# Kernel tuning notes

Hardware: AMD Instinct MI355X
Metric: run time of the kernel (lower is better)

The kernel has to match this reference:

```python
import jax, jax.numpy as jnp
import numpy as np

N_USER = 150_000
M_ITEM = 30_000
N_NODES = N_USER + M_ITEM
D = 64                      # embedding_dim
N_LAYERS = 3                # gcn_layer_number
E = 600_000                 # user-item interactions (symmetric nnz = 2E)
B = 1024
NUM_RATE, NUM_GENRE, NUM_DIR, NUM_ACT = 6, 25, 2186, 8030
NUM_GENDER, NUM_AGE, NUM_OCC, NUM_ZIP = 2, 7, 21, 3402
H1, H2 = 64, 64             # first/second fc hidden dims
FC1_IN = D * 10


def setup_inputs() -> dict:
    key = jax.random.key(0)
    ks = jax.random.split(key, 24)
    # aux features: 0/1 values are valid indices for every categorical field
    aux_info = jax.random.randint(ks[0], (B, 10246), 0, 2, dtype=jnp.int32)
    user_ids = jax.random.randint(ks[1], (B,), 0, N_USER, dtype=jnp.int32)
    item_ids = jax.random.randint(ks[2], (B,), 0, M_ITEM, dtype=jnp.int32)
    # bipartite graph: random interactions, symmetric normalized adjacency
    u = jax.random.randint(ks[3], (E,), 0, N_USER, dtype=jnp.int32)
    i = jax.random.randint(ks[4], (E,), 0, M_ITEM, dtype=jnp.int32) + N_USER
    graph_row = jnp.concatenate([u, i])
    graph_col = jnpph = jnp.concatenate([i, u]) if False else jnp.concatenate([i, u])
    deg = jax.ops.segment_sum(jnp.ones((2 * E,), jnp.float32), graph_row, num_segments=N_NODES)
    dinv = jnp.where(deg > 0, jax.lax.rsqrt(jnp.maximum(deg, 1.0)), 0.0)
    graph_val = dinv[graph_row] * dinv[graph_col]
    s = 0.1
    nrm = lambda k, shp: (jax.random.normal(k, shp, jnp.float32) * s)
    return {
        "aux_info": aux_info, "user_ids": user_ids, "item_ids": item_ids,
        "graph_row": graph_row, "graph_col": graph_col, "graph_val": graph_val,
        "rate_tab": nrm(ks[5], (NUM_RATE, D)),
        "genre_W": nrm(ks[6], (NUM_GENRE, D)),
        "director_W": nrm(ks[7], (NUM_DIR, D)),
        "actor_W": nrm(ks[8], (NUM_ACT, D)),
        "gender_tab": nrm(ks[9], (NUM_GENDER, D)),
        "age_tab": nrm(ks[10], (NUM_AGE, D)),
        "occ_tab": nrm(ks[11], (NUM_OCC, D)),
        "area_tab": nrm(ks[12], (NUM_ZIP, D)),
        "user_rel": nrm(ks[13], (N_USER, D)),
        "item_rel": nrm(ks[14], (M_ITEM, D)),
        "fc1_W": nrm(ks[15], (FC1_IN, H1)), "fc1_b": jnp.zeros((H1,), jnp.float32),
        "fc2_W": nrm(ks[16], (H1, H2)), "fc2_b": jnp.zeros((H2,), jnp.float32),
        "out_W": nrm(ks[17], (H2, 1)), "out_b": jnp.zeros((1,), jnp.float32),
    }


def _lightgcn(user_rel, item_rel, row, col, val):
    # LightGCN: repeated SpMM D^-1/2 A D^-1/2 @ emb, mean over layer outputs
    emb = jnp.concatenate([user_rel, item_rel], axis=0)      # [N, D]
    acc = emb
    for _ in range(N_LAYERS):
        emb = jax.ops.segment_sum(val[:, None] * emb[col], row, num_segments=N_NODES)
        acc = acc + emb
    light = acc / (N_LAYERS + 1)
    return light[:N_USER], light[N_USER:]


def _multi_hot(idx_int, W):
    x = idx_int.astype(jnp.float32)
    return (x @ W) / jnp.sum(x, axis=1, keepdims=True)


def reference(aux_info, user_ids, item_ids, graph_row, graph_col, graph_val,
              rate_tab, genre_W, director_W, actor_W,
              gender_tab, age_tab, occ_tab, area_tab,
              user_rel, item_rel,
              fc1_W, fc1_b, fc2_W, fc2_b, out_W, out_b):
    rate_idx = aux_info[:, 0]
    genre_idx = aux_info[:, 1:26]
    director_idx = aux_info[:, 26:2212]
    actor_idx = aux_info[:, 2212:10242]
    gender_idx = aux_info[:, 10242]
    age_idx = aux_info[:, 10243]
    occ_idx = aux_info[:, 10244]
    area_idx = aux_info[:, 10245]

    item_emb = jnp.concatenate([
        rate_tab[rate_idx],
        _multi_hot(genre_idx, genre_W),
        _multi_hot(director_idx, director_W),
        _multi_hot(actor_idx, actor_W),
    ], axis=1)                                               # [B, 4D]
    user_emb = jnp.concatenate([
        gender_tab[gender_idx], age_tab[age_idx],
        occ_tab[occ_idx], area_tab[area_idx],
    ], axis=1)                                               # [B, 4D]

    all_users, all_items = _lightgcn(user_rel, item_rel, graph_row, graph_col, graph_val)
    X = jnp.concatenate([item_emb, user_emb,
                         all_users[user_ids], all_items[item_ids]], axis=1)  # [B, 10D]
    X = jax.nn.relu(X @ fc1_W + fc1_b)
    X = jax.nn.relu(X @ fc2_W + fc2_b)
    return X @ out_W + out_b                                 # [B, 1]
```

## Files before the change

### kernel.cpp

```cpp
#include <hip/hip_runtime.h>
#include <hip/hip_bf16.h>
#include <hip/hip_fp16.h>

#define N_USER 150000
#define M_ITEM 30000
#define N_NODES 180000
#define E2 1200000
#define BATCH 1024
#define AUX_W 10246
#define KP_G 32
#define KP_D 2208
#define KP_A 8064
#define NBKT 265
#define WT_BLKS 2576
#define BCNT_BLKS 293

typedef __attribute__((ext_vector_type(8))) short short8;
typedef __attribute__((ext_vector_type(4))) float f32x4;

__device__ __forceinline__ int bucket_of(int r) {
    return r < N_USER ? (r >> 10) : 147 + ((r - N_USER) >> 8);
}

__device__ __forceinline__ int detect_f32(const void* probe) {
    float v = __bfloat162float(((const __hip_bfloat16*)probe)[threadIdx.x & 63]);
    unsigned long long m = __ballot(!(fabsf(v) < 1000.0f));
    return __popcll(m) > 8;
}

struct CvtSeg { const void* src; float* dst; int n; int blk0; };
struct CvtBatch { CvtSeg seg[16]; };

__global__ void __launch_bounds__(256) k_prep(CvtBatch cb, int cvtBlks,
                                              const void* Wg, const void* Wd, const void* Wa,
                                              unsigned short* WtG, unsigned short* WtD, unsigned short* WtA,
                                              const int* __restrict__ grow, int* __restrict__ bucket_tot,
                                              const void* probe) {
    int blk = blockIdx.x, tid = threadIdx.x;
    if (blk < cvtBlks) {
        int isf32 = detect_f32(probe);
        int si = 0;
        #pragma unroll
        for (int i = 0; i < 16; ++i) if (blk >= cb.seg[i].blk0) si = i;
        const CvtSeg sg = cb.seg[si];
        int i = (blk - sg.blk0) * 256 + tid;
        if (i >= sg.n) return;
        if (isf32) sg.dst[i] = ((const float*)sg.src)[i];
        else       sg.dst[i] = __bfloat162float(((const __hip_bfloat16*)sg.src)[i]);
        return;
    }
    if (blk < cvtBlks + WT_BLKS) {
        int isf32 = detect_f32(probe);
        int t = (blk - cvtBlks) * 256 + tid;
        if (t >= (KP_G + KP_D + KP_A) * 64) return;
        int kp = t >> 6, n = t & 63;
        int k, K; const void* src; unsigned short* dst;
        if (kp < KP_G)              { k = kp;               K = 25;   src = Wg; dst = WtG; }
        else if (kp < KP_G + KP_D)  { k = kp - KP_G;        K = 2186; src = Wd; dst = WtD; }
        else                        { k = kp - KP_G - KP_D; K = 8030; src = Wa; dst = WtA; }
        unsigned short v = 0;
        if (k < K) {
            if (isf32) {
                __hip_bfloat16 h = __float2bfloat16(((const float*)src)[(size_t)k * 64 + n]);
                v = *(unsigned short*)&h;
            } else {
                v = ((const unsigned short*)src)[(size_t)k * 64 + n];
            }
        }
        dst[(((size_t)(k >> 5) * 64 + n) * 4 + ((k >> 3) & 3)) * 8 + (k & 7)] = v;
        return;
    }
    __shared__ int h[NBKT];
    for (int i = tid; i < NBKT; i += 256) h[i] = 0;
    __syncthreads();
    int idx0 = (blk - cvtBlks - WT_BLKS) * 4096;
    #pragma unroll
    for (int k = 0; k < 16; ++k) {
        int i = idx0 + k * 256 + tid;
        if (i < E2) atomicAdd(&h[bucket_of(grow[i])], 1);
    }
    __syncthreads();
    for (int i = tid; i < NBKT; i += 256) if (h[i]) atomicAdd(&bucket_tot[i], h[i]);
}

__global__ void __launch_bounds__(512) k_bscan(const int* __restrict__ bucket_tot,
                                               int* __restrict__ bucket_base,
                                               int* __restrict__ bucketcur) {
    __shared__ int s[512];
    int tid = threadIdx.x;
    s[tid] = (tid < NBKT) ? bucket_tot[tid] : 0;
    __syncthreads();
    for (int off = 1; off < 512; off <<= 1) {
        int v = (tid >= off) ? s[tid - off] : 0;
        __syncthreads();
        s[tid] += v;
        __syncthreads();
    }
    int excl = tid ? s[tid - 1] : 0;
    bucket_base[tid] = excl;
    if (tid < NBKT) bucketcur[tid] = excl;
}

__global__ void __launch_bounds__(256) k_p1(const int* __restrict__ grow, const int* __restrict__ gcol,
                                            int* __restrict__ bucketcur, int2* __restrict__ binned) {
    __shared__ int h1[NBKT], base1[NBKT];
    int tid = threadIdx.x;
    for (int i = tid; i < NBKT; i += 256) h1[i] = 0;
    __syncthreads();
    int idx0 = blockIdx.x * 4096;
    int r[16], c[16];
    #pragma unroll
    for (int k = 0; k < 16; ++k) {
        int i = idx0 + k * 256 + tid;
        if (i < E2) {
            r[k] = grow[i]; c[k] = gcol[i];
            atomicAdd(&h1[bucket_of(r[k])], 1);
        } else r[k] = -1;
    }
    __syncthreads();
    for (int i = tid; i < NBKT; i += 256) {
        base1[i] = h1[i] ? atomicAdd(&bucketcur[i], h1[i]) : 0;
        h1[i] = 0;
    }
    __syncthreads();
    #pragma unroll
    for (int k = 0; k < 16; ++k) {
        if (r[k] >= 0) {
            int b = bucket_of(r[k]);
            int p = base1[b] + atomicAdd(&h1[b], 1);
            binned[p] = make_int2(r[k], c[k]);
        }
    }
}

__global__ void __launch_bounds__(256) k_p2(const int2* __restrict__ binned, const int* __restrict__ bb,
                                            int* __restrict__ cols, int2* __restrict__ moffs,
                                            float* __restrict__ dinv, float* __restrict__ dsq,
                                            float* __restrict__ gsc) {
    __shared__ int h[1024];
    __shared__ int ws2[256];
    int b = blockIdx.x, tid = threadIdx.x;
    int r0, r1;
    if (b < 147) { r0 = b << 10; r1 = min((b + 1) << 10, N_USER); }
    else         { r0 = N_USER + ((b - 147) << 8); r1 = min(N_USER + ((b - 146) << 8), N_NODES); }
    int s0 = bb[b], e0 = bb[b + 1];
    for (int i = tid; i < 1024; i += 256) h[i] = 0;
    __syncthreads();
    for (int j = s0 + tid; j < e0; j += 256) atomicAdd(&h[binned[j].x - r0], 1);
    __syncthreads();
    int t0 = tid * 4;
    int a0 = h[t0], a1 = h[t0 + 1], a2 = h[t0 + 2], a3 = h[t0 + 3];
    ws2[tid] = a0 + a1 + a2 + a3;
    __syncthreads();
    for (int off = 1; off < 256; off <<= 1) {
        int v = (tid >= off) ? ws2[tid - off] : 0;
        __syncthreads();
        ws2[tid] += v;
        __syncthreads();
    }
    int excl = tid ? ws2[tid - 1] : 0;
    int ex[4] = { excl, excl + a0, excl + a0 + a1, excl + a0 + a1 + a2 };
    int ac[4] = { a0, a1, a2, a3 };
    #pragma unroll
    for (int i = 0; i < 4; ++i) {
        int row = r0 + t0 + i;
        if (row < r1) {
            moffs[row] = make_int2(s0 + ex[i], s0 + ex[i] + ac[i]);
            float deg = (float)ac[i];
            bool nz = deg > 0.f;
            dinv[row] = nz ? rsqrtf(deg) : 0.f;
            dsq[row]  = nz ? 1.f / deg  : 0.f;
            gsc[row]  = nz ? sqrtf(deg) : 0.f;
        }
        h[t0 + i] = ex[i];
    }
    __syncthreads();
    for (int j = s0 + tid; j < e0; j += 256) {
        int2 e = binned[j];
        int p = s0 + atomicAdd(&h[e.x - r0], 1);
        cols[p] = e.y << 7;
    }
}

__device__ void mhgemm_body(int blk, const int* __restrict__ aux,
                            const unsigned short* __restrict__ WtG,
                            const unsigned short* __restrict__ WtD,
                            const unsigned short* __restrict__ WtA,
                            float* __restrict__ Xmh, float* __restrict__ cntf) {
    int seg, rb, k0, klen, Kseg, auxoff;
    const unsigned short* Wt;
    if (blk < 16)      { seg = 0; rb = blk;                      k0 = 0;              klen = 25;                  Kseg = 25;   auxoff = 1;    Wt = WtG; }
    else if (blk < 96) { int t = blk - 16; seg = 1; rb = t & 15; k0 = (t >> 4) * 512; klen = min(512, 2186 - k0); Kseg = 2186; auxoff = 26;   Wt = WtD; }
    else               { int t = blk - 96; seg = 2; rb = t & 15; k0 = (t >> 4) * 512; klen = min(512, 8030 - k0); Kseg = 8030; auxoff = 2212; Wt = WtA; }
    int lane = threadIdx.x & 63, wave = threadIdx.x >> 6;
    int m = lane & 15, quad = lane >> 4;
    int row = rb * 64 + wave * 16 + m;
    const int* arow = aux + (size_t)row * AUX_W + auxoff;

    f32x4 acc0 = {0.f,0.f,0.f,0.f}, acc1 = acc0, acc2 = acc0, acc3 = acc0;
    float asum = 0.f;
    int nchunk = (klen + 31) >> 5;
    for (int kci = 0; kci < nchunk; ++kci) {
        int kb = k0 + kci * 32 + quad * 8;
        short8 af;
        if (kb + 8 <= Kseg) {
            #pragma unroll
            for (int j = 0; j < 8; ++j) {
                int x = arow[kb + j];
                af[j] = x ? (short)0x3F80 : (short)0;
                asum += (float)x;
            }
        } else {
            #pragma unroll
            for (int j = 0; j < 8; ++j) {
                int x = (kb + j < Kseg) ? arow[kb + j] : 0;
                af[j] = x ? (short)0x3F80 : (short)0;
                asum += (float)x;
            }
        }
        size_t kcg = (size_t)(k0 >> 5) + kci;
        const unsigned short* bp = Wt + ((kcg * 64 + m) * 4 + quad) * 8;
        short8 b0 = *(const short8*)(bp);
        short8 b1 = *(const short8*)(bp + 512);
        short8 b2 = *(const short8*)(bp + 1024);
        short8 b3 = *(const short8*)(bp + 1536);
        acc0 = __builtin_amdgcn_mfma_f32_16x16x32_bf16(af, b0, acc0, 0, 0, 0);
        acc1 = __builtin_amdgcn_mfma_f32_16x16x32_bf16(af, b1, acc1, 0, 0, 0);
        acc2 = __builtin_amdgcn_mfma_f32_16x16x32_bf16(af, b2, acc2, 0, 0, 0);
        acc3 = __builtin_amdgcn_mfma_f32_16x16x32_bf16(af, b3, acc3, 0, 0, 0);
    }
    asum += __shfl_xor(asum, 16);
    asum += __shfl_xor(asum, 32);
    if (quad == 0) atomicAdd(&cntf[seg * BATCH + row], asum);
    float* xbase = Xmh + ((size_t)seg * BATCH + rb * 64 + wave * 16 + quad * 4) * 64;
    #pragma unroll
    for (int reg = 0; reg < 4; ++reg) {
        float* xr = xbase + (size_t)reg * 64;
        atomicAdd(&xr[ 0 + m], acc0[reg]);
        atomicAdd(&xr[16 + m], acc1[reg]);
        atomicAdd(&xr[32 + m], acc2[reg]);
        atomicAdd(&xr[48 + m], acc3[reg]);
    }
}

__global__ void __launch_bounds__(256) k_cvt_fused(const void* rawU, const void* rawI,
                                                   const float* __restrict__ dinv,
                                                   __half* __restrict__ emb,
                                                   float* __restrict__ tacc,
                                                   const int* __restrict__ uids,
                                                   const int* __restrict__ iids, int cvtN,
                                                   const int2* __restrict__ moffs,
                                                   const int* __restrict__ cols,
                                                   int2* __restrict__ moffs2,
                                                   const int* __restrict__ aux,
                                                   const unsigned short* __restrict__ WtG,
                                                   const unsigned short* __restrict__ WtD,
                                                   const unsigned short* __restrict__ WtA,
                                                   float* __restrict__ Xmh, float* __restrict__ cntf) {
    int blk = blockIdx.x;
    if (blk < 352) {
        mhgemm_body(blk, aux, WtG, WtD, WtA, Xmh, cntf);
        return;
    }
    if (blk < 864) {
        int lane = threadIdx.x & 63;
        int t = (blk - 352) * 4 + (threadIdx.x >> 6);
        int r = (t < BATCH) ? uids[t] : (N_USER + iids[t - BATCH]);
        int2 se = moffs[r];
        if (lane == 0) moffs2[r] = se;
        for (int j = se.x + lane; j < se.y; j += 64) {
            int c = (unsigned)cols[j] >> 7;
            moffs2[c] = moffs[c];
        }
        return;
    }
    int isf32 = detect_f32(rawU);
    if (blk < 1376) {
        int lane = threadIdx.x & 63;
        int t = (blk - 864) * 4 + (threadIdx.x >> 6);
        const void* src; size_t ri;
        if (t < BATCH) { src = rawU; ri = (size_t)uids[t]; }
        else           { src = rawI; ri = (size_t)iids[t - BATCH]; }
        float v;
        if (isf32) v = ((const float*)src)[ri * 64 + lane];
        else       v = __bfloat162float(((const __hip_bfloat16*)src)[ri * 64 + lane]);
        tacc[(size_t)t * 64 + lane] = v;
        return;
    }
    int q = (blk - 1376) * 256 + threadIdx.x;
    if (q >= N_NODES * 16) return;
    int r = q >> 4;
    const void* src; size_t qq;
    if (r < N_USER) { src = rawU; qq = (size_t)q; }
    else            { src = rawI; qq = (size_t)q - (size_t)N_USER * 16; }
    float d = dinv[r];
    float4 v;
    if (isf32) {
        v = ((const float4*)src)[qq];
    } else {
        ushort4 u = ((const ushort4*)src)[qq];
        v.x = __bfloat162float(*(__hip_bfloat16*)&u.x);
        v.y = __bfloat162float(*(__hip_bfloat16*)&u.y);
        v.z = __bfloat162float(*(__hip_bfloat16*)&u.z);
        v.w = __bfloat162float(*(__hip_bfloat16*)&u.w);
    }
    __half h0 = __float2half(v.x * d), h1 = __float2half(v.y * d);
    __half h2 = __float2half(v.z * d), h3 = __float2half(v.w * d);
    ushort4 o = { *(unsigned short*)&h0, *(unsigned short*)&h1,
                  *(unsigned short*)&h2, *(unsigned short*)&h3 };
    ((ushort4*)emb)[(size_t)q] = o;
}

__global__ void __launch_bounds__(256, 8) k_spmv(const __half* __restrict__ src, __half* __restrict__ dst,
                                                 const int2* __restrict__ moffs_in, const int* __restrict__ cols,
                                                 const float* __restrict__ dsq,
                                                 int spmvN, float* __restrict__ tacc,
                                                 const int* __restrict__ uids, const int* __restrict__ iids,
                                                 const float* __restrict__ gsc) {
    int tid = threadIdx.x, lane = tid & 63;
    int blk = blockIdx.x;
    if (blk >= spmvN) {
        int t = (blk - spmvN) * 4 + (tid >> 6);
        int r = (t < BATCH) ? uids[t] : (N_USER + iids[t - BATCH]);
        tacc[(size_t)t * 64 + lane] += __half2float(src[(size_t)r * 64 + lane]) * gsc[r];
        return;
    }
    int wid = blk * 4 + (tid >> 6);
    if (wid >= N_NODES) return;
    int2 se = moffs_in[wid];
    int s = se.x, e = se.y;
    if (e <= s) return;
    int p = lane & 31, ep = lane >> 5;
    const char* sb = (const char*)src + (p << 2);
    float ax = 0.f, ay = 0.f;
    int j0 = s;
    for (; j0 + 16 <= e; j0 += 16) {
        int c[8];
        #pragma unroll
        for (int u = 0; u < 8; ++u) c[u] = cols[j0 + 2 * u + ep];
        float2 v[8];
        #pragma unroll
        for (int u = 0; u < 8; ++u) v[u] = __half22float2(*(const __half2*)(sb + (size_t)(unsigned)c[u]));
        #pragma unroll
        for (int u = 0; u < 8; ++u) { ax += v[u].x; ay += v[u].y; }
    }
    if (j0 + 8 <= e) {
        int c[4];
        #pragma unroll
        for (int u = 0; u < 4; ++u) c[u] = cols[j0 + 2 * u + ep];
        float2 v[4];
        #pragma unroll
        for (int u = 0; u < 4; ++u) v[u] = __half22float2(*(const __half2*)(sb + (size_t)(unsigned)c[u]));
        #pragma unroll
        for (int u = 0; u < 4; ++u) { ax += v[u].x; ay += v[u].y; }
        j0 += 8;
    }
    if (j0 + 4 <= e) {
        int c0 = cols[j0 + ep], c1 = cols[j0 + 2 + ep];
        float2 v0 = __half22float2(*(const __half2*)(sb + (size_t)(unsigned)c0));
        float2 v1 = __half22float2(*(const __half2*)(sb + (size_t)(unsigned)c1));
        ax += v0.x + v1.x; ay += v0.y + v1.y;
        j0 += 4;
    }
    if (j0 < e) {
        int j1 = j0 + ep, j2 = j0 + 2 + ep;
        int c0 = cols[min(j1, e - 1)], c1 = cols[min(j2, e - 1)];
        float w0 = (j1 < e) ? 1.f : 0.f, w1 = (j2 < e) ? 1.f : 0.f;
        float2 v0 = __half22float2(*(const __half2*)(sb + (size_t)(unsigned)c0));
        float2 v1 = __half22float2(*(const __half2*)(sb + (size_t)(unsigned)c1));
        ax = fmaf(w0, v0.x, ax); ay = fmaf(w0, v0.y, ay);
        ax = fmaf(w1, v1.x, ax); ay = fmaf(w1, v1.y, ay);
    }
    ax += __shfl_xor(ax, 32);
    ay += __shfl_xor(ay, 32);
    if (ep == 0) {
        float d = dsq[wid];
        *(__half2*)((char*)dst + ((size_t)wid << 7) + (p << 2)) = __floats2half2_rn(ax * d, ay * d);
    }
}

__global__ void __launch_bounds__(256) k_spmv3(const __half* __restrict__ src, float* __restrict__ tacc,
                                               const int2* __restrict__ moffs, const int* __restrict__ cols,
                                               const float* __restrict__ dinv, const float* __restrict__ gsc,
                                               const int* __restrict__ uids, const int* __restrict__ iids) {
    int tid = threadIdx.x, lane = tid & 63;
    int t = blockIdx.x * 4 + (tid >> 6);
    if (t >= 2048) return;
    int r = (t < BATCH) ? uids[t] : (N_USER + iids[t - BATCH]);
    int2 se = moffs[r];
    int s = se.x, e = se.y;
    int p = lane & 31, ep = lane >> 5;
    const char* sb = (const char*)src + (p << 2);
    float ax = 0.f, ay = 0.f;
    int j0 = s;
    for (; j0 + 16 <= e; j0 += 16) {
        int c[8];
        #pragma unroll
        for (int u = 0; u < 8; ++u) c[u] = cols[j0 + 2 * u + ep];
        float2 v[8];
        #pragma unroll
        for (int u = 0; u < 8; ++u) v[u] = __half22float2(*(const __half2*)(sb + (size_t)(unsigned)c[u]));
        #pragma unroll
        for (int u = 0; u < 8; ++u) { ax += v[u].x; ay += v[u].y; }
    }
    if (j0 + 8 <= e) {
        int c[4];
        #pragma unroll
        for (int u = 0; u < 4; ++u) c[u] = cols[j0 + 2 * u + ep];
        float2 v[4];
        #pragma unroll
        for (int u = 0; u < 4; ++u) v[u] = __half22float2(*(const __half2*)(sb + (size_t)(unsigned)c[u]));
        #pragma unroll
        for (int u = 0; u < 4; ++u) { ax += v[u].x; ay += v[u].y; }
        j0 += 8;
    }
    if (j0 + 4 <= e) {
        int c0 = cols[j0 + ep], c1 = cols[j0 + 2 + ep];
        float2 v0 = __half22float2(*(const __half2*)(sb + (size_t)(unsigned)c0));
        float2 v1 = __half22float2(*(const __half2*)(sb + (size_t)(unsigned)c1));
        ax += v0.x + v1.x; ay += v0.y + v1.y;
        j0 += 4;
    }
    if (j0 < e) {
        int j1 = j0 + ep, j2 = j0 + 2 + ep;
        int c0 = cols[min(j1, e - 1)], c1 = cols[min(j2, e - 1)];
        float w0 = (j1 < e) ? 1.f : 0.f, w1 = (j2 < e) ? 1.f : 0.f;
        float2 v0 = __half22float2(*(const __half2*)(sb + (size_t)(unsigned)c0));
        float2 v1 = __half22float2(*(const __half2*)(sb + (size_t)(unsigned)c1));
        ax = fmaf(w0, v0.x, ax); ay = fmaf(w0, v0.y, ay);
        ax = fmaf(w1, v1.x, ax); ay = fmaf(w1, v1.y, ay);
    }
    ax += __shfl_xor(ax, 32);
    ay += __shfl_xor(ay, 32);
    if (ep == 0) {
        float2 self = __half22float2(*(const __half2*)((const char*)src + ((size_t)r << 7) + (p << 2)));
        float di = dinv[r], g = gsc[r];
        float* tp = tacc + (size_t)t * 64 + (p << 1);
        tp[0] += di * ax + g * self.x;
        tp[1] += di * ay + g * self.y;
    }
}

__global__ void __launch_bounds__(256) k_mlp(const int* __restrict__ aux,
                                             const float* __restrict__ ratef, const float* __restrict__ genderf,
                                             const float* __restrict__ agef, const float* __restrict__ occf,
                                             const float* __restrict__ areaf, const float* __restrict__ tacc,
                                             const float* __restrict__ Xmh, const float* __restrict__ cntf,
                                             const float* __restrict__ W1, const float* __restrict__ b1,
                                             const float* __restrict__ W2, const float* __restrict__ b2,
                                             const float* __restrict__ Wo, const float* __restrict__ bo,
                                             void* __restrict__ out, const void* probe) {
    __shared__ float sx[4][640];
    __shared__ float sh[4][64];
    int isf32 = detect_f32(probe);
    int lane = threadIdx.x & 63, w = threadIdx.x >> 6;
    int b = blockIdx.x * 4 + w;
    const int* arow = aux + (size_t)b * AUX_W;
    float* xr = sx[w];
    xr[0   + lane] = ratef[arow[0] * 64 + lane];
    xr[64  + lane] = Xmh[((size_t)0 * BATCH + b) * 64 + lane] / cntf[0 * BATCH + b];
    xr[128 + lane] = Xmh[((size_t)1 * BATCH + b) * 64 + lane] / cntf[1 * BATCH + b];
    xr[192 + lane] = Xmh[((size_t)2 * BATCH + b) * 64 + lane] / cntf[2 * BATCH + b];
    xr[256 + lane] = genderf[arow[10242] * 64 + lane];
    xr[320 + lane] = agef[arow[10243] * 64 + lane];
    xr[384 + lane] = occf[arow[10244] * 64 + lane];
    xr[448 + lane] = areaf[arow[10245] * 64 + lane];
    xr[512 + lane] = tacc[(size_t)b * 64 + lane] * 0.25f;
    xr[576 + lane] = tacc[(size_t)(BATCH + b) * 64 + lane] * 0.25f;
    float acc = b1[lane];
    #pragma unroll 8
    for (int k = 0; k < 640; ++k) acc += xr[k] * W1[(size_t)k * 64 + lane];
    float h1 = fmaxf(acc, 0.f);
    sh[w][lane] = h1;
    float acc2 = b2[lane];
    #pragma unroll 8
    for (int j = 0; j < 64; ++j) acc2 += sh[w][j] * W2[(size_t)j * 64 + lane];
    float h2 = fmaxf(acc2, 0.f);
    float p = h2 * Wo[lane];
    #pragma unroll
    for (int off = 32; off; off >>= 1) p += __shfl_down(p, off);
    if (lane == 0) {
        float r = p + bo[0];
        if (isf32) ((float*)out)[b] = r;
        else       ((__hip_bfloat16*)out)[b] = __float2bfloat16(r);
    }
}

extern "C" void kernel_launch(void* const* d_in, const int* in_sizes, int n_in,
                              void* d_out, int out_size, void* d_ws, size_t ws_size,
                              hipStream_t stream) {
    const int* aux  = (const int*)d_in[0];
    const int* uids = (const int*)d_in[1];
    const int* iids = (const int*)d_in[2];
    const int* grow = (const int*)d_in[3];
    const int* gcol = (const int*)d_in[4];

    char* p = (char*)d_ws;
    auto alloc = [&](size_t bytes) -> char* {
        char* r = p;
        p += (bytes + 255) / 256 * 256;
        return r;
    };
    int*   bucket_tot  = (int*)alloc(512 * 4);
    float* Xmh         = (float*)alloc((size_t)3 * BATCH * 64 * 4);
    float* cntf        = (float*)alloc((size_t)3 * BATCH * 4);
    int2*  moffs2      = (int2*)alloc((size_t)180224 * 8);
    char*  zero_end    = p;
    int*   bucket_base = (int*)alloc(512 * 4);
    int*   bucketcur   = (int*)alloc(512 * 4);
    int2*  moffs       = (int2*)alloc((size_t)180224 * 8);
    float* dinv        = (float*)alloc((size_t)180224 * 4);
    float* dsq         = (float*)alloc((size_t)180224 * 4);
    float* gsc         = (float*)alloc((size_t)180224 * 4);
    int2*  binned      = (int2*)alloc((size_t)E2 * 8);
    int*   cols        = (int*)alloc((size_t)E2 * 4);
    __half* embA       = (__half*)alloc((size_t)N_NODES * 64 * 2);
    __half* embB       = (__half*)alloc((size_t)N_NODES * 64 * 2);
    float* tacc        = (float*)alloc((size_t)2048 * 64 * 4);
    unsigned short* WtG = (unsigned short*)alloc((size_t)KP_G * 64 * 2);
    unsigned short* WtD = (unsigned short*)alloc((size_t)KP_D * 64 * 2);
    unsigned short* WtA = (unsigned short*)alloc((size_t)KP_A * 64 * 2);
    float* ratef   = (float*)alloc(384 * 4);
    float* genderf = (float*)alloc(128 * 4);
    float* agef    = (float*)alloc(448 * 4);
    float* occf    = (float*)alloc(1344 * 4);
    float* areaf   = (float*)alloc((size_t)217728 * 4);
    float* fc1W    = (float*)alloc((size_t)40960 * 4);
    float* fc1b    = (float*)alloc(64 * 4);
    float* fc2W    = (float*)alloc(4096 * 4);
    float* fc2b    = (float*)alloc(64 * 4);
    float* outW    = (float*)alloc(64 * 4);
    float* outb    = (float*)alloc(4);

    const void* probe = d_in[14];

    hipMemsetAsync(bucket_tot, 0, (size_t)(zero_end - (char*)bucket_tot), stream);

    CvtBatch cb;
    int blk = 0, si = 0;
    auto addseg = [&](const void* s, float* d, int n) {
        cb.seg[si].src = s; cb.seg[si].dst = d; cb.seg[si].n = n; cb.seg[si].blk0 = blk;
        blk += (n + 255) / 256; ++si;
    };
    addseg(d_in[6],  ratef,   384);
    addseg(d_in[10], genderf, 128);
    addseg(d_in[11], agef,    448);
    addseg(d_in[12], occf,    1344);
    addseg(d_in[13], areaf,   217728);
    addseg(d_in[16], fc1W,   40960);
    addseg(d_in[17], fc1b,   64);
    addseg(d_in[18], fc2W,   4096);
    addseg(d_in[19], fc2b,   64);
    addseg(d_in[20], outW,   64);
    addseg(d_in[21], outb,   1);
    for (int i = si; i < 16; ++i) { cb.seg[i].src = nullptr; cb.seg[i].dst = nullptr; cb.seg[i].n = 0; cb.seg[i].blk0 = 0x7fffffff; }
    const int cvtBlks = blk;
    hipLaunchKernelGGL(k_prep, dim3(cvtBlks + WT_BLKS + BCNT_BLKS), dim3(256), 0, stream,
                       cb, cvtBlks, d_in[7], d_in[8], d_in[9], WtG, WtD, WtA, grow, bucket_tot, probe);

    hipLaunchKernelGGL(k_bscan, dim3(1), dim3(512), 0, stream, bucket_tot, bucket_base, bucketcur);
    hipLaunchKernelGGL(k_p1, dim3((E2 + 4095) / 4096), dim3(256), 0, stream, grow, gcol, bucketcur, binned);
    hipLaunchKernelGGL(k_p2, dim3(NBKT), dim3(256), 0, stream, binned, bucket_base, cols, moffs, dinv, dsq, gsc);

    const int cvtN = (N_NODES * 16 + 255) / 256;
    hipLaunchKernelGGL(k_cvt_fused, dim3(1376 + cvtN), dim3(256), 0, stream,
                       d_in[14], d_in[15], dinv, embA, tacc, uids, iids, cvtN,
                       moffs, cols, moffs2, aux, WtG, WtD, WtA, Xmh, cntf);

    const int spmvN = (N_NODES + 3) / 4;
    hipLaunchKernelGGL(k_spmv, dim3(spmvN), dim3(256), 0, stream,
                       embA, embB, moffs, cols, dsq, spmvN, (float*)nullptr, uids, iids, gsc);
    hipLaunchKernelGGL(k_spmv, dim3(spmvN + 512), dim3(256), 0, stream,
                       embB, embA, moffs2, cols, dsq, spmvN, tacc, uids, iids, gsc);
    hipLaunchKernelGGL(k_spmv3, dim3(2048 / 4), dim3(256), 0, stream,
                       embA, tacc, moffs, cols, dinv, gsc, uids, iids);

    hipLaunchKernelGGL(k_mlp, dim3(BATCH / 4), dim3(256), 0, stream,
                       aux, ratef, genderf, agef, occf, areaf, tacc, Xmh, cntf,
                       fc1W, fc1b, fc2W, fc2b, outW, outb, d_out, probe);
}
```

Baseline: 335.0 us.

## Map eight rows per wavefront in SpMV with 16-byte gathers

The SpMV kernel now assigns eight graph rows to each 64-lane wavefront, with eight lanes per row each loading a 16-byte chunk (eight halves) of a neighbour embedding. This replaces the one-row-per-wave scheme that used 4-byte loads split across two half-waves plus a cross-lane shuffle. The goal is to cut wave count and use wider vector gathers, so idle lanes on short rows (average degree is about 6-7) are reduced. The tradeoff is that rows with very different degrees inside one wave can diverge, and the grid size assumes N_NODES divides evenly by 32.

```diff
diff --git a/kernel.cpp b/kernel.cpp
--- a/kernel.cpp
+++ b/kernel.cpp
@@ -325,57 +325,61 @@
         tacc[(size_t)t * 64 + lane] += __half2float(src[(size_t)r * 64 + lane]) * gsc[r];
         return;
     }
-    int wid = blk * 4 + (tid >> 6);
-    if (wid >= N_NODES) return;
-    int2 se = moffs_in[wid];
+    int wid8 = blk * 4 + (tid >> 6);
+    int g = lane >> 3, l8 = lane & 7;
+    int r = wid8 * 8 + g;
+    int2 se = moffs_in[r];
     int s = se.x, e = se.y;
-    if (e <= s) return;
-    int p = lane & 31, ep = lane >> 5;
-    const char* sb = (const char*)src + (p << 2);
-    float ax = 0.f, ay = 0.f;
+    const char* sb = (const char*)src + (l8 << 4);
+    float2 a0 = {0.f,0.f}, a1 = a0, a2 = a0, a3 = a0;
     int j0 = s;
-    for (; j0 + 16 <= e; j0 += 16) {
-        int c[8];
-        #pragma unroll
-        for (int u = 0; u < 8; ++u) c[u] = cols[j0 + 2 * u + ep];
-        float2 v[8];
-        #pragma unroll
-        for (int u = 0; u < 8; ++u) v[u] = __half22float2(*(const __half2*)(sb + (size_t)(unsigned)c[u]));
-        #pragma unroll
-        for (int u = 0; u < 8; ++u) { ax += v[u].x; ay += v[u].y; }
-    }
-    if (j0 + 8 <= e) {
+    for (; j0 + 4 <= e; j0 += 4) {
         int c[4];
         #pragma unroll
-        for (int u = 0; u < 4; ++u) c[u] = cols[j0 + 2 * u + ep];
-        float2 v[4];
-        #pragma unroll
-        for (int u = 0; u < 4; ++u) v[u] = __half22float2(*(const __half2*)(sb + (size_t)(unsigned)c[u]));
-        #pragma unroll
-        for (int u = 0; u < 4; ++u) { ax += v[u].x; ay += v[u].y; }
-        j0 += 8;
-    }
-    if (j0 + 4 <= e) {
-        int c0 = cols[j0 + ep], c1 = cols[j0 + 2 + ep];
-        float2 v0 = __half22float2(*(const __half2*)(sb + (size_t)(unsigned)c0));
-        float2 v1 = __half22float2(*(const __half2*)(sb + (size_t)(unsigned)c1));
-        ax += v0.x + v1.x; ay += v0.y + v1.y;
-        j0 += 4;
+        for (int u = 0; u < 4; ++u) c[u] = cols[j0 + u];
+        float4 rv[4];
+        #pragma unroll
+        for (int u = 0; u < 4; ++u) rv[u] = *(const float4*)(sb + (size_t)(unsigned)c[u]);
+        #pragma unroll
+        for (int u = 0; u < 4; ++u) {
+            const __half2* h = (const __half2*)&rv[u];
+            float2 f0 = __half22float2(h[0]), f1 = __half22float2(h[1]);
+            float2 f2 = __half22float2(h[2]), f3 = __half22float2(h[3]);
+            a0.x += f0.x; a0.y += f0.y; a1.x += f1.x; a1.y += f1.y;
+            a2.x += f2.x; a2.y += f2.y; a3.x += f3.x; a3.y += f3.y;
+        }
     }
     if (j0 < e) {
-        int j1 = j0 + ep, j2 = j0 + 2 + ep;
-        int c0 = cols[min(j1, e - 1)], c1 = cols[min(j2, e - 1)];
-        float w0 = (j1 < e) ? 1.f : 0.f, w1 = (j2 < e) ? 1.f : 0.f;
-        float2 v0 = __half22float2(*(const __half2*)(sb + (size_t)(unsigned)c0));
-        float2 v1 = __half22float2(*(const __half2*)(sb + (size_t)(unsigned)c1));
-        ax = fmaf(w0, v0.x, ax); ay = fmaf(w0, v0.y, ay);
-        ax = fmaf(w1, v1.x, ax); ay = fmaf(w1, v1.y, ay);
-    }
-    ax += __shfl_xor(ax, 32);
-    ay += __shfl_xor(ay, 32);
-    if (ep == 0) {
-        float d = dsq[wid];
-        *(__half2*)((char*)dst + ((size_t)wid << 7) + (p << 2)) = __floats2half2_rn(ax * d, ay * d);
+        int c[4]; float w[4];
+        #pragma unroll
+        for (int u = 0; u < 4; ++u) {
+            int j = j0 + u;
+            c[u] = cols[min(j, e - 1)];
+            w[u] = (j < e) ? 1.f : 0.f;
+        }
+        float4 rv[4];
+        #pragma unroll
+        for (int u = 0; u < 4; ++u) rv[u] = *(const float4*)(sb + (size_t)(unsigned)c[u]);
+        #pragma unroll
+        for (int u = 0; u < 4; ++u) {
+            const __half2* h = (const __half2*)&rv[u];
+            float2 f0 = __half22float2(h[0]), f1 = __half22float2(h[1]);
+            float2 f2 = __half22float2(h[2]), f3 = __half22float2(h[3]);
+            a0.x = fmaf(w[u], f0.x, a0.x); a0.y = fmaf(w[u], f0.y, a0.y);
+            a1.x = fmaf(w[u], f1.x, a1.x); a1.y = fmaf(w[u], f1.y, a1.y);
+            a2.x = fmaf(w[u], f2.x, a2.x); a2.y = fmaf(w[u], f2.y, a2.y);
+            a3.x = fmaf(w[u], f3.x, a3.x); a3.y = fmaf(w[u], f3.y, a3.y);
+        }
+    }
+    if (e > s) {
+        float d = dsq[r];
+        float4 ov;
+        __half2* op = (__half2*)&ov;
+        op[0] = __floats2half2_rn(a0.x * d, a0.y * d);
+        op[1] = __floats2half2_rn(a1.x * d, a1.y * d);
+        op[2] = __floats2half2_rn(a2.x * d, a2.y * d);
+        op[3] = __floats2half2_rn(a3.x * d, a3.y * d);
+        *(float4*)((char*)dst + ((size_t)r << 7) + (l8 << 4)) = ov;
     }
 }
 
@@ -567,7 +571,7 @@
                        d_in[14], d_in[15], dinv, embA, tacc, uids, iids, cvtN,
                        moffs, cols, moffs2, aux, WtG, WtD, WtA, Xmh, cntf);
 
-    const int spmvN = (N_NODES + 3) / 4;
+    const int spmvN = N_NODES / 32;
     hipLaunchKernelGGL(k_spmv, dim3(spmvN), dim3(256), 0, stream,
                        embA, embB, moffs, cols, dsq, spmvN, (float*)nullptr, uids, iids, gsc);
     hipLaunchKernelGGL(k_spmv, dim3(spmvN + 512), dim3(256), 0, stream,
```

New measurement: 302.3 us. -9.8%, faster.
